# Kernel tuning notes

Measured on AMD Instinct MI355X. Metric: run time of the kernel, lower is better.

The kernel has to match this reference:

```python
import jax, jax.numpy as jnp
import numpy as np
from jax import lax

B, T, N = 256, 2048, 64  # batch, max_seq_len, num_tags


def setup_inputs() -> dict:
    key = jax.random.key(0)
    k1, k2, k3 = jax.random.split(key, 3)
    x = jax.random.normal(k1, (B, T, N), dtype=jnp.float32)
    seq_len = jax.random.randint(k2, (B,), 1, T + 1).astype(jnp.int32)
    trans = (jax.random.normal(k3, (N, N), dtype=jnp.float32) * 0.1)
    return {"x": x, "seq_len": seq_len, "trans": trans}


def reference(x, seq_len, trans):
    # Viterbi decode (tfa.text.crf_decode): returns (tags [B,T] int32, scores [B] float)
    Bv, Tv, Nv = x.shape
    alpha0 = x[:, 0]                                   # [B,N]
    xs = jnp.swapaxes(x[:, 1:], 0, 1)                  # [T-1,B,N]
    valid = jnp.arange(1, Tv)[:, None] < seq_len[None, :]  # [T-1,B]
    ident = jnp.arange(Nv, dtype=jnp.int32)

    def fwd(alpha, inp):
        x_t, v = inp
        # scores[b, prev, cur] = alpha[b, prev] + trans[prev, cur]
        sc = alpha[:, :, None] + trans[None]           # [B,N,N]
        bp = jnp.argmax(sc, axis=1).astype(jnp.int32)  # [B,N] best prev tag per cur
        new_alpha = jnp.max(sc, axis=1) + x_t          # [B,N]
        # steps beyond seq_len: carry state, identity backpointer
        alpha_n = jnp.where(v[:, None], new_alpha, alpha)
        bp = jnp.where(v[:, None], bp, ident[None, :])
        return alpha_n, bp

    alpha_f, bps = lax.scan(fwd, alpha0, (xs, valid))  # bps: [T-1,B,N]
    scores = jnp.max(alpha_f, axis=-1)                 # [B]
    last = jnp.argmax(alpha_f, axis=-1).astype(jnp.int32)  # [B] tag at last step

    def bwd(tag, bp):
        prev = jnp.take_along_axis(bp, tag[:, None], axis=1)[:, 0]
        return prev, tag  # emit tag at step t+1, carry tag at step t

    first, rest = lax.scan(bwd, last, bps, reverse=True)   # rest: [T-1,B]
    tags = jnp.concatenate([first[:, None], jnp.swapaxes(rest, 0, 1)], axis=1)  # [B,T]
    return tags, scores
```

## Files before the change

### kernel.cpp

```cpp
#include <hip/hip_runtime.h>

#define BB 256
#define TT 2048
#define NN 64

template <int K>
__device__ __forceinline__ int rot_i(int v) {
  return __builtin_amdgcn_update_dpp(0, v, 0x120 | K, 0xF, 0xF, true);
}
template <int K>
__device__ __forceinline__ float rot_f(float v) {
  return __int_as_float(rot_i<K>(__float_as_int(v)));
}
__device__ __forceinline__ void pswap16(int &a, int &b) {
  asm volatile("v_permlane16_swap_b32 %0, %1" : "+v"(a), "+v"(b));
}
__device__ __forceinline__ void pswap32(int &a, int &b) {
  asm volatile("v_permlane32_swap_b32 %0, %1" : "+v"(a), "+v"(b));
}
__device__ __forceinline__ float pair16_max(float m) {
  int a = __float_as_int(m), b = a;
  pswap16(a, b);
  return fmaxf(__int_as_float(a), __int_as_float(b));
}
__device__ __forceinline__ float pair32_max(float m) {
  int a = __float_as_int(m), b = a;
  pswap32(a, b);
  return fmaxf(__int_as_float(a), __int_as_float(b));
}
__device__ __forceinline__ int pair16_min(int v) {
  int a = v, b = v;
  pswap16(a, b);
  return a < b ? a : b;
}
__device__ __forceinline__ int pair32_min(int v) {
  int a = v, b = v;
  pswap32(a, b);
  return a < b ? a : b;
}
__device__ __forceinline__ float wave_max64(float v) {
  float m = v;
  m = fmaxf(m, rot_f<8>(m));
  m = fmaxf(m, rot_f<4>(m));
  m = fmaxf(m, rot_f<2>(m));
  m = fmaxf(m, rot_f<1>(m));
  m = pair16_max(m);
  m = pair32_max(m);
  return m;
}

__global__ __launch_bounds__(64, 1)
void crf_viterbi_fast(const float* __restrict__ x,
                      const int* __restrict__ seq_len,
                      const float* __restrict__ trans,
                      float* __restrict__ out,
                      float* __restrict__ hist) {
  const int b = blockIdx.x;
  const int lane = threadIdx.x;

  __shared__ float transT[NN * 65];

  const float* xb = x + (size_t)b * TT * NN;
  float* hb = hist + (size_t)b * TT * NN;
  const int slen = seq_len[b];
  const int bTT = b * TT;

  for (int r = 0; r < NN; ++r) transT[lane * 65 + r] = trans[r * NN + lane];

  float tc0[16], tc1[16], tc2[16], tc3[16];
  {
    int s = lane;
    tc0[0] = trans[s * NN + lane];
    tc1[0] = trans[(s ^ 16) * NN + lane];
    tc2[0] = trans[(s ^ 32) * NN + lane];
    tc3[0] = trans[(s ^ 48) * NN + lane];
  }
#define TCL(K) { int s = rot_i<K>(lane);            \
    tc0[K] = trans[s * NN + lane];                   \
    tc1[K] = trans[(s ^ 16) * NN + lane];            \
    tc2[K] = trans[(s ^ 32) * NN + lane];            \
    tc3[K] = trans[(s ^ 48) * NN + lane]; }
  TCL(1) TCL(2) TCL(3) TCL(4) TCL(5) TCL(6) TCL(7) TCL(8)
  TCL(9) TCL(10) TCL(11) TCL(12) TCL(13) TCL(14) TCL(15)
#undef TCL

  float av = xb[lane];
  hb[lane] = av;
  float xn1 = xb[NN + lane];
  float xn2 = xb[2 * NN + lane];
  float xn3 = xb[3 * NN + lane];

  for (int t = 1; t < slen; ++t) {
    float xv = xn1; xn1 = xn2; xn2 = xn3;
    {
      int tn = (t + 3 < TT) ? (t + 3) : (TT - 1);
      xn3 = xb[(size_t)tn * NN + lane];
    }

    float w1 = __shfl_xor(av, 16, 64);
    float w2 = __shfl_xor(av, 32, 64);
    float w3 = __shfl_xor(av, 48, 64);

#define Q(K) fmaxf(fmaxf(rot_f<K>(av) + tc0[K], rot_f<K>(w1) + tc1[K]), \
                   fmaxf(rot_f<K>(w2) + tc2[K], rot_f<K>(w3) + tc3[K]))
    float m0 = fmaxf(fmaxf(av + tc0[0], w1 + tc1[0]),
                     fmaxf(w2 + tc2[0], w3 + tc3[0]));
    float m1 = Q(1), m2 = Q(2), m3 = Q(3);
    m0 = fmaxf(m0, Q(4));  m1 = fmaxf(m1, Q(5));
    m2 = fmaxf(m2, Q(6));  m3 = fmaxf(m3, Q(7));
    m0 = fmaxf(m0, Q(8));  m1 = fmaxf(m1, Q(9));
    m2 = fmaxf(m2, Q(10)); m3 = fmaxf(m3, Q(11));
    m0 = fmaxf(m0, Q(12)); m1 = fmaxf(m1, Q(13));
    m2 = fmaxf(m2, Q(14)); m3 = fmaxf(m3, Q(15));
#undef Q
    float m = fmaxf(fmaxf(m0, m1), fmaxf(m2, m3));
    av = m + xv;

    hb[(size_t)t * NN + lane] = av;
  }

  const float best = wave_max64(av);
  const int last = ((int)__builtin_ctzll(__ballot(av == best))) & 63;

  for (int t = slen - 1 + lane; t < TT; t += NN) out[bTT + t] = (float)last;
  if (lane == 0) out[BB * TT + b] = best;

  int start = slen - 2;
  if (start >= 0) {
    asm volatile("s_waitcnt vmcnt(0)" ::: "memory");
    int tag = last;
#define LDR(ROW) hb[(size_t)(((ROW) > 0) ? (ROW) : 0) * NN + lane]
    float r0 = LDR(start), r1 = LDR(start - 1), r2 = LDR(start - 2),
          r3 = LDR(start - 3);
    int t = start;
#define TSTEP(RREG, TIDX) {                                            \
      float val = (RREG) + transT[tag * 65 + lane];                    \
      float mm = wave_max64(val);                                      \
      tag = ((int)__builtin_ctzll(__ballot(val == mm))) & 63;          \
      if (lane == 0) out[bTT + (TIDX)] = (float)tag;                   \
    }
    while (t >= 3) {
      TSTEP(r0, t);     r0 = LDR(t - 4);
      TSTEP(r1, t - 1); r1 = LDR(t - 5);
      TSTEP(r2, t - 2); r2 = LDR(t - 6);
      TSTEP(r3, t - 3); r3 = LDR(t - 7);
      t -= 4;
    }
    if (t >= 0) TSTEP(r0, t);
    if (t >= 1) TSTEP(r1, t - 1);
    if (t >= 2) TSTEP(r2, t - 2);
#undef TSTEP
#undef LDR
  }
}

__global__ __launch_bounds__(256, 1)
void crf_viterbi_fb(const float* __restrict__ x,
                    const int* __restrict__ seq_len,
                    const float* __restrict__ trans,
                    float* __restrict__ out) {
  const int b = blockIdx.x;
  const int tid = threadIdx.x;
  const int lane = tid & 63;
  const int w = tid >> 6;
  const int c = lane & 15;
  const int jc = (w << 4) + c;

  __shared__ __align__(16) float alpha_s[2][NN];
  __shared__ unsigned char bp_s[(TT - 1) * NN];
  __shared__ int map_s[4][NN];

  const float* xb = x + (size_t)b * TT * NN;
  const int slen = seq_len[b];

  int idxv[16];
  idxv[0] = lane;
  idxv[1] = rot_i<1>(lane);   idxv[2] = rot_i<2>(lane);
  idxv[3] = rot_i<3>(lane);   idxv[4] = rot_i<4>(lane);
  idxv[5] = rot_i<5>(lane);   idxv[6] = rot_i<6>(lane);
  idxv[7] = rot_i<7>(lane);   idxv[8] = rot_i<8>(lane);
  idxv[9] = rot_i<9>(lane);   idxv[10] = rot_i<10>(lane);
  idxv[11] = rot_i<11>(lane); idxv[12] = rot_i<12>(lane);
  idxv[13] = rot_i<13>(lane); idxv[14] = rot_i<14>(lane);
  idxv[15] = rot_i<15>(lane);

  float tcv[16];
#pragma unroll
  for (int k = 0; k < 16; ++k) tcv[k] = trans[idxv[k] * NN + jc];

  if (w == 0) alpha_s[0][lane] = xb[lane];
  __syncthreads();

  float xn1 = xb[NN + jc];
  float xn2 = xb[2 * NN + jc];

  for (int t = 1; t < slen; ++t) {
    float xv = xn1;
    xn1 = xn2;
    {
      int tn = (t + 2 < TT) ? (t + 2) : (TT - 1);
      xn2 = xb[(size_t)tn * NN + jc];
    }
    const int pr = (t + 1) & 1;
    const int pw = t & 1;

    float avf = alpha_s[pr][lane];

    float c0 = avf + tcv[0];
    float c1 = rot_f<1>(avf) + tcv[1];
    float c2 = rot_f<2>(avf) + tcv[2];
    float c3 = rot_f<3>(avf) + tcv[3];
    float c4 = rot_f<4>(avf) + tcv[4];
    float c5 = rot_f<5>(avf) + tcv[5];
    float c6 = rot_f<6>(avf) + tcv[6];
    float c7 = rot_f<7>(avf) + tcv[7];
    float c8 = rot_f<8>(avf) + tcv[8];
    float c9 = rot_f<9>(avf) + tcv[9];
    float c10 = rot_f<10>(avf) + tcv[10];
    float c11 = rot_f<11>(avf) + tcv[11];
    float c12 = rot_f<12>(avf) + tcv[12];
    float c13 = rot_f<13>(avf) + tcv[13];
    float c14 = rot_f<14>(avf) + tcv[14];
    float c15 = rot_f<15>(avf) + tcv[15];

    float m = fmaxf(fmaxf(fmaxf(fmaxf(c0, c1), fmaxf(c2, c3)),
                          fmaxf(fmaxf(c4, c5), fmaxf(c6, c7))),
                    fmaxf(fmaxf(fmaxf(c8, c9), fmaxf(c10, c11)),
                          fmaxf(fmaxf(c12, c13), fmaxf(c14, c15))));
    m = pair16_max(m);
    m = pair32_max(m);

    int s0 = (c0 == m) ? idxv[0] : NN;
    int s1 = (c1 == m) ? idxv[1] : NN;
    int s2 = (c2 == m) ? idxv[2] : NN;
    int s3 = (c3 == m) ? idxv[3] : NN;
    int s4 = (c4 == m) ? idxv[4] : NN;
    int s5 = (c5 == m) ? idxv[5] : NN;
    int s6 = (c6 == m) ? idxv[6] : NN;
    int s7 = (c7 == m) ? idxv[7] : NN;
    int s8 = (c8 == m) ? idxv[8] : NN;
    int s9 = (c9 == m) ? idxv[9] : NN;
    int s10 = (c10 == m) ? idxv[10] : NN;
    int s11 = (c11 == m) ? idxv[11] : NN;
    int s12 = (c12 == m) ? idxv[12] : NN;
    int s13 = (c13 == m) ? idxv[13] : NN;
    int s14 = (c14 == m) ? idxv[14] : NN;
    int s15 = (c15 == m) ? idxv[15] : NN;
    int idx = min(min(min(min(s0, s1), min(s2, s3)),
                      min(min(s4, s5), min(s6, s7))),
                  min(min(min(s8, s9), min(s10, s11)),
                      min(min(s12, s13), min(s14, s15))));
    idx = pair16_min(idx);
    idx = pair32_min(idx);

    if (lane < 16) {
      alpha_s[pw][jc] = m + xv;
      bp_s[(t - 1) * NN + jc] = (unsigned char)idx;
    }
    asm volatile("s_waitcnt lgkmcnt(0)\n\ts_barrier" ::: "memory");
  }

  const int pf = (slen - 1) & 1;
  float best = alpha_s[pf][lane];
  int last = lane;
#pragma unroll
  for (int mask = 1; mask < 64; mask <<= 1) {
    float ov = __shfl_xor(best, mask, 64);
    int oi = __shfl_xor(last, mask, 64);
    bool take = (ov > best) || (ov == best && oi < last);
    best = take ? ov : best;
    last = take ? oi : last;
  }
  const float lastf = (float)last;
  const int bTT = b * TT;

  for (int t = slen - 1 + tid; t < TT; t += 256) out[bTT + t] = lastf;
  if (tid == 0) out[BB * TT + b] = best;

  const int lo = 512 * w;
  const int hi = ((512 * (w + 1) - 1) < (slen - 2)) ? (512 * (w + 1) - 1)
                                                    : (slen - 2);
  if (w > 0) {
    int s = lane;
    for (int r = hi; r >= lo; --r) s = bp_s[r * NN + s];
    map_s[w][lane] = s;
  }
  __syncthreads();

  const int e3 = last;
  const int e2 = map_s[3][e3];
  const int e1 = map_s[2][e2];
  const int e0 = map_s[1][e1];
  const int entry = (w == 3) ? e3 : (w == 2) ? e2 : (w == 1) ? e1 : e0;

  if (lane == 0) {
    int s = entry;
    for (int r = hi; r >= lo; --r) {
      s = bp_s[r * NN + s];
      out[bTT + r] = (float)s;
    }
  }
}

extern "C" void kernel_launch(void* const* d_in, const int* in_sizes, int n_in,
                              void* d_out, int out_size, void* d_ws, size_t ws_size,
                              hipStream_t stream) {
  const float* x = (const float*)d_in[0];
  const int* seq_len = (const int*)d_in[1];
  const float* trans = (const float*)d_in[2];
  float* out = (float*)d_out;

  const size_t need = (size_t)BB * TT * NN * sizeof(float);
  if (ws_size >= need) {
    crf_viterbi_fast<<<BB, 64, 0, stream>>>(x, seq_len, trans, out,
                                            (float*)d_ws);
  } else {
    crf_viterbi_fb<<<BB, 256, 0, stream>>>(x, seq_len, trans, out);
  }
}
```

Baseline: 887.3 us.

## Broadcast alpha through double-buffered LDS float4 reads instead of DPP rotations

```diff
diff --git a/kernel.cpp b/kernel.cpp
--- a/kernel.cpp
+++ b/kernel.cpp
@@ -58,6 +58,7 @@
   const int b = blockIdx.x;
   const int lane = threadIdx.x;
 
+  __shared__ __align__(16) float alpha_s[2][NN];
   __shared__ float transT[NN * 65];
 
   const float* xb = x + (size_t)b * TT * NN;
@@ -67,56 +68,68 @@
 
   for (int r = 0; r < NN; ++r) transT[lane * 65 + r] = trans[r * NN + lane];
 
-  float tc0[16], tc1[16], tc2[16], tc3[16];
-  {
-    int s = lane;
-    tc0[0] = trans[s * NN + lane];
-    tc1[0] = trans[(s ^ 16) * NN + lane];
-    tc2[0] = trans[(s ^ 32) * NN + lane];
-    tc3[0] = trans[(s ^ 48) * NN + lane];
-  }
-#define TCL(K) { int s = rot_i<K>(lane);            \
-    tc0[K] = trans[s * NN + lane];                   \
-    tc1[K] = trans[(s ^ 16) * NN + lane];            \
-    tc2[K] = trans[(s ^ 32) * NN + lane];            \
-    tc3[K] = trans[(s ^ 48) * NN + lane]; }
-  TCL(1) TCL(2) TCL(3) TCL(4) TCL(5) TCL(6) TCL(7) TCL(8)
-  TCL(9) TCL(10) TCL(11) TCL(12) TCL(13) TCL(14) TCL(15)
-#undef TCL
+  float tc[NN];
+#pragma unroll
+  for (int i = 0; i < NN; ++i) tc[i] = trans[i * NN + lane];
+#pragma unroll
+  for (int i = 0; i < NN; ++i) asm volatile("" : "+v"(tc[i]));
 
   float av = xb[lane];
   hb[lane] = av;
+  alpha_s[0][lane] = av;
   float xn1 = xb[NN + lane];
   float xn2 = xb[2 * NN + lane];
   float xn3 = xb[3 * NN + lane];
 
+  int cur = 0;
   for (int t = 1; t < slen; ++t) {
+    asm volatile("" ::: "memory");
+
     float xv = xn1; xn1 = xn2; xn2 = xn3;
     {
       int tn = (t + 3 < TT) ? (t + 3) : (TT - 1);
       xn3 = xb[(size_t)tn * NN + lane];
     }
 
-    float w1 = __shfl_xor(av, 16, 64);
-    float w2 = __shfl_xor(av, 32, 64);
-    float w3 = __shfl_xor(av, 48, 64);
-
-#define Q(K) fmaxf(fmaxf(rot_f<K>(av) + tc0[K], rot_f<K>(w1) + tc1[K]), \
-                   fmaxf(rot_f<K>(w2) + tc2[K], rot_f<K>(w3) + tc3[K]))
-    float m0 = fmaxf(fmaxf(av + tc0[0], w1 + tc1[0]),
-                     fmaxf(w2 + tc2[0], w3 + tc3[0]));
-    float m1 = Q(1), m2 = Q(2), m3 = Q(3);
-    m0 = fmaxf(m0, Q(4));  m1 = fmaxf(m1, Q(5));
-    m2 = fmaxf(m2, Q(6));  m3 = fmaxf(m3, Q(7));
-    m0 = fmaxf(m0, Q(8));  m1 = fmaxf(m1, Q(9));
-    m2 = fmaxf(m2, Q(10)); m3 = fmaxf(m3, Q(11));
-    m0 = fmaxf(m0, Q(12)); m1 = fmaxf(m1, Q(13));
-    m2 = fmaxf(m2, Q(14)); m3 = fmaxf(m3, Q(15));
-#undef Q
+    const float* as = alpha_s[cur];
+    float m0, m1, m2, m3;
+    {
+      float4 a0 = *reinterpret_cast<const float4*>(as + 0);
+      float4 a1 = *reinterpret_cast<const float4*>(as + 16);
+      float4 a2 = *reinterpret_cast<const float4*>(as + 32);
+      float4 a3 = *reinterpret_cast<const float4*>(as + 48);
+      m0 = fmaxf(fmaxf(a0.x + tc[0],  a0.y + tc[1]),
+                 fmaxf(a0.z + tc[2],  a0.w + tc[3]));
+      m1 = fmaxf(fmaxf(a1.x + tc[16], a1.y + tc[17]),
+                 fmaxf(a1.z + tc[18], a1.w + tc[19]));
+      m2 = fmaxf(fmaxf(a2.x + tc[32], a2.y + tc[33]),
+                 fmaxf(a2.z + tc[34], a2.w + tc[35]));
+      m3 = fmaxf(fmaxf(a3.x + tc[48], a3.y + tc[49]),
+                 fmaxf(a3.z + tc[50], a3.w + tc[51]));
+    }
+#define BLK(K4)                                                          \
+    {                                                                    \
+      float4 a0 = *reinterpret_cast<const float4*>(as + (K4));           \
+      float4 a1 = *reinterpret_cast<const float4*>(as + 16 + (K4));      \
+      float4 a2 = *reinterpret_cast<const float4*>(as + 32 + (K4));      \
+      float4 a3 = *reinterpret_cast<const float4*>(as + 48 + (K4));      \
+      m0 = fmaxf(m0, fmaxf(fmaxf(a0.x + tc[(K4) + 0],  a0.y + tc[(K4) + 1]),  \
+                           fmaxf(a0.z + tc[(K4) + 2],  a0.w + tc[(K4) + 3])));\
+      m1 = fmaxf(m1, fmaxf(fmaxf(a1.x + tc[(K4) + 16], a1.y + tc[(K4) + 17]), \
+                           fmaxf(a1.z + tc[(K4) + 18], a1.w + tc[(K4) + 19])));\
+      m2 = fmaxf(m2, fmaxf(fmaxf(a2.x + tc[(K4) + 32], a2.y + tc[(K4) + 33]), \
+                           fmaxf(a2.z + tc[(K4) + 34], a2.w + tc[(K4) + 35])));\
+      m3 = fmaxf(m3, fmaxf(fmaxf(a3.x + tc[(K4) + 48], a3.y + tc[(K4) + 49]), \
+                           fmaxf(a3.z + tc[(K4) + 50], a3.w + tc[(K4) + 51])));\
+    }
+    BLK(4) BLK(8) BLK(12)
+#undef BLK
     float m = fmaxf(fmaxf(m0, m1), fmaxf(m2, m3));
     av = m + xv;
 
+    alpha_s[cur ^ 1][lane] = av;
     hb[(size_t)t * NN + lane] = av;
+    cur ^= 1;
   }
 
   const float best = wave_max64(av);
```

Result: no change. 900.3 us (+1.5%).
